# Kernel tuning notes

Measured on AMD Instinct MI355X. Metric: run time of the kernel, lower is better.

Reference implementation:

```python
import jax, jax.numpy as jnp
import numpy as np

B, C, N = 16, 256, 2048
CK = int(C * 0.25)  # key/query channels = 64
CV = C              # value_size = 1 -> value channels = C
BN_EPS = 1e-5


def setup_inputs() -> dict:
    key = jax.random.key(0)
    ks = jax.random.split(key, 7)
    sq = lambda fan_in: 1.0 / np.sqrt(fan_in)
    x = jax.random.normal(ks[0], (B, C, N), dtype=jnp.float32)
    # Conv1d(kernel_size=1, bias=False) weights stored as [out_ch, in_ch]
    Wq = jax.random.uniform(ks[1], (CK, C), jnp.float32, -sq(C), sq(C))
    Wk = jax.random.uniform(ks[2], (CK, C), jnp.float32, -sq(C), sq(C))
    Wv = jax.random.uniform(ks[3], (CV, C), jnp.float32, -sq(C), sq(C))
    Wl = jax.random.uniform(ks[4], (C, C), jnp.float32, -sq(C), sq(C))
    gamma = jnp.ones((C,), jnp.float32)
    beta = jnp.zeros((C,), jnp.float32)
    return {"x": x, "Wq": Wq, "Wk": Wk, "Wv": Wv, "Wl": Wl,
            "gamma": gamma, "beta": beta}


def reference(x, Wq, Wk, Wv, Wl, gamma, beta):
    # x: [B, C, N]
    q = jnp.einsum('oc,bcn->bno', Wq, x)   # [B, N, CK]  (q_conv then permute)
    k = jnp.einsum('oc,bcn->bon', Wk, x)   # [B, CK, N]
    v = jnp.einsum('oc,bcn->bno', Wv, x)   # [B, N, CV]  (v_conv then permute)

    w = jnp.einsum('bnk,bkm->bnm', q, k)   # [B, N, N] raw logits
    # NOTE: column-sum divisor uses RAW logits (RHS evaluated before reassignment
    # in the torch source), not the softmax output.
    col_sum = w.sum(axis=1, keepdims=True)                 # [B, 1, N]
    s = jax.nn.softmax(w, axis=-1) / (1e-9 + col_sum)      # [B, N, N]

    att = jnp.einsum('bnm,bmc->bcn', s, v)  # [B, C, N] (matmul + permute back)
    r = x - att                              # offset (residual of attention)

    # lbr: 1x1 conv -> BatchNorm1d (training-mode batch stats) -> ReLU
    h = jnp.einsum('oc,bcn->bon', Wl, r)     # [B, C, N]
    mean = h.mean(axis=(0, 2), keepdims=True)
    var = ((h - mean) ** 2).mean(axis=(0, 2), keepdims=True)  # biased, as BN
    hn = (h - mean) * jax.lax.rsqrt(var + BN_EPS)
    bn = hn * gamma[None, :, None] + beta[None, :, None]
    out = x + jax.nn.relu(bn)
    return out
```

## Files before the change

kernel.cpp:

```cpp
#include <hip/hip_runtime.h>

#define B_ 16
#define C_ 256
#define N_ 2048
#define CK_ 64

using f32x4  = __attribute__((ext_vector_type(4))) float;
using bf16x8 = __attribute__((ext_vector_type(8))) short;
using short4_t = __attribute__((ext_vector_type(4))) short;
using u32x2  = __attribute__((ext_vector_type(2))) unsigned;

static __device__ __forceinline__ float bf2f(short s){
  unsigned u = ((unsigned)(unsigned short)s) << 16;
  float f; __builtin_memcpy(&f, &u, 4); return f;
}
static __device__ __forceinline__ short f2bf(float f){
  unsigned u; __builtin_memcpy(&u, &f, 4);
  unsigned r = (u + 0x7fffu + ((u >> 16) & 1u)) >> 16;
  return (short)(unsigned short)r;
}

static __device__ __forceinline__ int vf_off(int cp, int ck){
  int q = cp >> 1; int ch = (((cp & 1) << 2) | ck) ^ (q & 7);
  return q*128 + ch*16;
}

__global__ void k_prep(const float* __restrict__ Wq, const float* __restrict__ Wk,
                       const float* __restrict__ Wv, const float* __restrict__ Wl,
                       short* __restrict__ Wb, short* __restrict__ Wlf,
                       const float* __restrict__ x, double* __restrict__ xsum){
  int bid = blockIdx.x;
  if(bid < 1024){
    int b = bid >> 6;
    int c = (bid & 63)*4 + (threadIdx.x>>6);
    int l = threadIdx.x & 63;
    const float* row = x + ((size_t)b*C_ + c)*N_;
    double s = 0.0;
    #pragma unroll
    for(int it = 0; it < 8; ++it){
      f32x4 v = *(const f32x4*)(row + it*256 + l*4);
      s += (double)v[0] + (double)v[1] + (double)v[2] + (double)v[3];
    }
    for(int off = 32; off; off >>= 1) s += __shfl_down(s, off);
    if(l == 0) xsum[b*C_ + c] = s;
  } else {
    int i = (bid - 1024)*256 + threadIdx.x;
    if(i < 384*C_){
      int o = i >> 8;
      float v;
      if(o < 64)       v = Wq[i];
      else if(o < 128) v = Wk[i - 64*C_];
      else             v = Wv[i - 128*C_];
      Wb[i] = f2bf(v);
    }
    if(i < C_*C_){
      int o = i >> 8, c = i & 255;
      int dest = (c>>5)*8192 + (o>>4)*512 + ((((c>>3)&3)*16) + (o&15))*8 + (c&7);
      Wlf[dest] = f2bf(Wl[i]);
    }
  }
}

__global__ void k_prep_g2(const double* __restrict__ xsum, const float* __restrict__ Wq,
                          const float* __restrict__ Wk, double* __restrict__ g){
  int b = blockIdx.x;
  __shared__ double xs[C_];
  __shared__ double t[CK_];
  int tid = threadIdx.x;
  xs[tid] = xsum[b*C_ + tid];
  __syncthreads();
  if(tid < CK_){
    double s = 0.0;
    const float* wr = Wq + (size_t)tid*C_;
    for(int c = 0; c < C_; ++c) s += (double)wr[c]*xs[c];
    t[tid] = s;
  }
  __syncthreads();
  double s = 0.0;
  for(int j = 0; j < CK_; ++j) s += (double)Wk[(size_t)j*C_ + tid]*t[j];
  g[b*C_ + tid] = s;
}

#define XROW 328
__global__ __launch_bounds__(256,2) void k_qkv(const float* __restrict__ x,
        const short* __restrict__ Wb, const double* __restrict__ gg,
        short* __restrict__ qbuf, short* __restrict__ kf, short* __restrict__ vf,
        short* __restrict__ xTb){
  int b = blockIdx.y; int n0 = blockIdx.x*64;
  int tid = threadIdx.x, w = tid>>6, l = tid&63, lo = l&15, g = l>>4;
  __shared__ __attribute__((aligned(16))) short xT[64*XROW];
  __shared__ double gs[C_];
  __shared__ double csum2[256][4];
  __shared__ float inv_lds[64];
  const float* xb = x + (size_t)b*C_*N_;
  gs[tid] = gg[b*C_ + tid];
  __syncthreads();
  int pp2 = tid >> 4, cg = tid & 15;
  double cs[4] = {0.0, 0.0, 0.0, 0.0};
  #pragma unroll
  for(int cc = 0; cc < 8; ++cc){
    int ci = cc*32 + 2*pp2;
    f32x4 x0 = *(const f32x4*)(xb + (size_t)ci*N_ + n0 + 4*cg);
    f32x4 x1 = *(const f32x4*)(xb + (size_t)(ci+1)*N_ + n0 + 4*cg);
    #pragma unroll
    for(int jq = 0; jq < 4; ++jq){
      cs[jq] += (double)x0[jq]*gs[ci] + (double)x1[jq]*gs[ci+1];
      unsigned pr = (unsigned)(unsigned short)f2bf(x0[jq])
                  | (((unsigned)(unsigned short)f2bf(x1[jq]))<<16);
      *(unsigned*)(&xT[(4*cg + jq)*XROW + cc*40 + 2*pp2]) = pr;
    }
  }
  csum2[tid][0] = cs[0]; csum2[tid][1] = cs[1];
  csum2[tid][2] = cs[2]; csum2[tid][3] = cs[3];
  __syncthreads();
  if(tid < 64){
    int cgq = tid >> 2, jq = tid & 3;
    double tot = 0.0;
    #pragma unroll
    for(int k = 0; k < 16; ++k) tot += csum2[k*16 + cgq][jq];
    inv_lds[tid] = (float)(1.0/(1e-9 + tot));
  }

  f32x4 acc[6][4];
  #pragma unroll
  for(int oi=0;oi<6;++oi) for(int nj=0;nj<4;++nj) acc[oi][nj]=(f32x4){0.f,0.f,0.f,0.f};
  int n2 = tid>>2, ii2 = tid&3;
  short* xtb = xTb + ((size_t)b*N_ + n0)*C_;
  #pragma unroll
  for(int cc = 0; cc < 8; ++cc){
    *(bf16x8*)(xtb + (size_t)n2*C_ + cc*32 + 8*ii2) =
        *(const bf16x8*)(&xT[n2*XROW + cc*40 + 8*ii2]);
    bf16x8 bfr[4];
    #pragma unroll
    for(int nj = 0; nj < 4; ++nj)
      bfr[nj] = *(const bf16x8*)(&xT[(nj*16 + lo)*XROW + cc*40 + 8*g]);
    #pragma unroll
    for(int oi = 0; oi < 6; ++oi){
      int o = w*96 + oi*16 + lo;
      bf16x8 af = *(const bf16x8*)(Wb + (size_t)o*C_ + cc*32 + 8*g);
      #pragma unroll
      for(int nj = 0; nj < 4; ++nj)
        acc[oi][nj] = __builtin_amdgcn_mfma_f32_16x16x32_bf16(af, bfr[nj], acc[oi][nj], 0,0,0);
    }
  }
  __syncthreads();

  short* qb  = qbuf + (size_t)b*N_*64;
  short* kfb = kf   + (size_t)b*N_*64;
  short* vfb = vf   + (size_t)b*C_*N_;
  #pragma unroll
  for(int oi = 0; oi < 6; ++oi){
    int obase = w*96 + oi*16;
    for(int nj = 0; nj < 4; ++nj){
      int n = n0 + nj*16 + lo;
      if(obase < 64){
        short4_t pk;
        #pragma unroll
        for(int r = 0; r < 4; ++r) pk[r] = f2bf(acc[oi][nj][r]);
        *(short4_t*)(qb + (size_t)n*64 + obase + 4*g) = pk;
      } else if(obase < 128){
        int C0 = obase - 64 + 4*g;
        int mt = (n0>>4) + nj;
        int h  = C0 >> 5;
        int lanep = ((C0>>3)&3)*16 + lo;
        short4_t pk;
        #pragma unroll
        for(int r = 0; r < 4; ++r) pk[r] = f2bf(acc[oi][nj][r]);
        *(short4_t*)(kfb + ((size_t)(mt*2 + h)*64 + lanep)*8 + (C0&4)) = pk;
      } else {
        float iv = inv_lds[nj*16 + lo];
        int ckk = (n>>3)&3, wi = n&7, mc = n>>5;
        #pragma unroll
        for(int r = 0; r < 4; ++r){
          int cp = obase - 128 + 4*g + r;
          vfb[(size_t)mc*8192 + (vf_off(cp, ckk)>>1) + wi] = f2bf(acc[oi][nj][r]*iv);
        }
      }
    }
  }
}
#undef XROW

__global__ __launch_bounds__(256,2) void k_attn(const short* __restrict__ qbuf,
        const short* __restrict__ kf, const short* __restrict__ vf,
        short* __restrict__ att){
  int d = blockIdx.x;
  int xcd = d & 7, j = d >> 3;
  int b = xcd*2 + (j >> 5);
  int n0 = (j & 31)*64;
  int tid = threadIdx.x;
  int w = tid>>6, l = tid&63, lo = l&15, g = l>>4;

  __shared__ short vlds[2][16384];
  __shared__ short plds[4096];
  __shared__ float rs_lds[64];

  const short* qb  = qbuf + (size_t)b*N_*64;
  const short* kfb = kf   + (size_t)b*N_*64;
  const short* vfb = vf   + (size_t)b*C_*N_;

  bf16x8 qa0, qa1;
  {
    const short* qrow = qb + (size_t)(n0 + w*16 + lo)*64;
    qa0 = *(const bf16x8*)(qrow + 8*g);
    qa1 = *(const bf16x8*)(qrow + 32 + 8*g);
  }
  int paoff[4][2], bvoff[4][2], pw[4];
  #pragma unroll
  for(int rt = 0; rt < 4; ++rt)
    #pragma unroll
    for(int mh = 0; mh < 2; ++mh)
      paoff[rt][mh] = (rt*16 + lo)*128 + (((mh*4 + g) ^ (lo&7))*16);
  #pragma unroll
  for(int jj = 0; jj < 4; ++jj)
    #pragma unroll
    for(int mh = 0; mh < 2; ++mh)
      bvoff[jj][mh] = mh*16384 + vf_off(w*64 + jj*16 + lo, g);
  #pragma unroll
  for(int tt = 0; tt < 4; ++tt)
    pw[tt] = (w*16 + lo)*128 + (((tt*2 + (g>>1)) ^ (lo&7))*16) + (g&1)*8;

  const short* kl   = kfb + l*8;
  const short* vsrc = vfb + w*2048 + l*8;

  f32x4 oacc[4][4];
  #pragma unroll
  for(int rt=0;rt<4;++rt) for(int jj=0;jj<4;++jj) oacc[rt][jj]=(f32x4){0.f,0.f,0.f,0.f};
  float srow = 0.f;

  bf16x8 kA0,kA1,kA2,kA3,kA4,kA5,kA6,kA7;
  bf16x8 kB0,kB1,kB2,kB3,kB4,kB5,kB6,kB7;

#define LOADK(S, MC) { const short* kp = kl + (size_t)((MC)&31)*4096; \
    k##S##0 = *(const bf16x8*)(kp);        k##S##1 = *(const bf16x8*)(kp + 512); \
    k##S##2 = *(const bf16x8*)(kp + 1024); k##S##3 = *(const bf16x8*)(kp + 1536); \
    k##S##4 = *(const bf16x8*)(kp + 2048); k##S##5 = *(const bf16x8*)(kp + 2560); \
    k##S##6 = *(const bf16x8*)(kp + 3072); k##S##7 = *(const bf16x8*)(kp + 3584); }
#define GLLDS(SRC, DST) __builtin_amdgcn_global_load_lds( \
    (const __attribute__((address_space(1))) void*)(SRC), \
    (__attribute__((address_space(3))) void*)(DST), 16, 0, 0)
#define VDMA(MC, NB) { const short* vs = vsrc + (size_t)(2*(MC))*8192; \
    char* dst = (char*)&vlds[NB][0] + w*4096; \
    GLLDS(vs,        dst);        GLLDS(vs +  512, dst + 1024); \
    GLLDS(vs + 1024, dst + 2048); GLLDS(vs + 1536, dst + 3072); \
    GLLDS(vs + 8192,  dst + 16384); GLLDS(vs + 8704,  dst + 17408); \
    GLLDS(vs + 9216,  dst + 18432); GLLDS(vs + 9728,  dst + 19456); }
#define QKT(S, TT, KE, KO) { \
    f32x4 a = (f32x4){0.f,0.f,0.f,0.f}; \
    a = __builtin_amdgcn_mfma_f32_16x16x32_bf16(k##S##KE, qa0, a, 0,0,0); \
    a = __builtin_amdgcn_mfma_f32_16x16x32_bf16(k##S##KO, qa1, a, 0,0,0); \
    float e[4]; \
    _Pragma("unroll") \
    for(int r = 0; r < 4; ++r) e[r] = __builtin_exp2f(fmaf(a[r], 1.44269504f, -17.3123405f)); \
    srow += e[0]+e[1]+e[2]+e[3]; \
    unsigned p0, p1; \
    asm("v_cvt_pk_bf16_f32 %0, %1, %2" : "=v"(p0) : "v"(e[0]), "v"(e[1])); \
    asm("v_cvt_pk_bf16_f32 %0, %1, %2" : "=v"(p1) : "v"(e[2]), "v"(e[3])); \
    { u32x2 pv = {p0, p1}; *(u32x2*)((char*)&plds[0] + pw[TT]) = pv; } }

  LOADK(A, 0);
  LOADK(B, 1);
  VDMA(0, 0);

#define BODY(BUF, S, MC) { \
    VDMA(((MC)+1)&31, (BUF)^1); \
    QKT(S, 0, 0, 1); QKT(S, 1, 2, 3); QKT(S, 2, 4, 5); QKT(S, 3, 6, 7); \
    LOADK(S, (MC)+2); \
    __builtin_amdgcn_sched_barrier(0); \
    asm volatile("s_waitcnt vmcnt(16) lgkmcnt(0)" ::: "memory"); \
    __builtin_amdgcn_s_barrier(); \
    __builtin_amdgcn_sched_barrier(0); \
    __builtin_amdgcn_s_setprio(1); \
    _Pragma("unroll") \
    for(int mh = 0; mh < 2; ++mh){ \
      bf16x8 pa[4], bv[4]; \
      _Pragma("unroll") \
      for(int rt = 0; rt < 4; ++rt) pa[rt] = *(const bf16x8*)((char*)&plds[0] + paoff[rt][mh]); \
      _Pragma("unroll") \
      for(int jj = 0; jj < 4; ++jj) bv[jj] = *(const bf16x8*)((char*)&vlds[BUF][0] + bvoff[jj][mh]); \
      _Pragma("unroll") \
      for(int rt = 0; rt < 4; ++rt) \
        _Pragma("unroll") \
        for(int jj = 0; jj < 4; ++jj) \
          oacc[rt][jj] = __builtin_amdgcn_mfma_f32_16x16x32_bf16(pa[rt], bv[jj], oacc[rt][jj], 0,0,0); \
    } \
    __builtin_amdgcn_s_setprio(0); \
    __builtin_amdgcn_sched_barrier(0); \
    asm volatile("s_waitcnt lgkmcnt(0)" ::: "memory"); \
    __builtin_amdgcn_s_barrier(); \
    __builtin_amdgcn_sched_barrier(0); }

  #pragma unroll 1
  for(int it = 0; it < 16; ++it){
    BODY(0, A, 2*it);
    BODY(1, B, 2*it + 1);
  }
#undef BODY
#undef QKT
#undef VDMA
#undef GLLDS
#undef LOADK

  float S = srow;
  S += __shfl_xor(S, 16);
  S += __shfl_xor(S, 32);
  if(l < 16) rs_lds[w*16 + l] = 1.f/(S + 1e-30f);
  __syncthreads();
  float rinvs[4][4];
  #pragma unroll
  for(int rt = 0; rt < 4; ++rt)
    #pragma unroll
    for(int r = 0; r < 4; ++r) rinvs[rt][r] = rs_lds[rt*16 + 4*g + r];

  short* attb = att + (size_t)b*N_*C_;
  #pragma unroll
  for(int rt = 0; rt < 4; ++rt)
    #pragma unroll
    for(int jj = 0; jj < 4; ++jj)
      #pragma unroll
      for(int r = 0; r < 4; ++r){
        int n = n0 + rt*16 + 4*g + r;
        int c = w*64 + jj*16 + lo;
        attb[(size_t)n*C_ + c] = f2bf(oacc[rt][jj][r]*rinvs[rt][r]);
      }
}

__global__ __launch_bounds__(256,2) void k_hgemm(const short* __restrict__ xTb,
        const short* __restrict__ att, const short* __restrict__ Wlf,
        short* __restrict__ hT, float* __restrict__ part){
  int b = blockIdx.y; int n0 = blockIdx.x*64;
  int bid = b*32 + blockIdx.x;
  int tid = threadIdx.x, w = tid>>6, l = tid&63, lo = l&15, g = l>>4;
  __shared__ __attribute__((aligned(16))) short rT[64*C_];
  const short* xtb = xTb + ((size_t)b*N_ + n0)*C_;
  const short* atb = att + ((size_t)b*N_ + n0)*C_;
  int half = l >> 5, ch = l & 31;
  #pragma unroll
  for(int k = 0; k < 8; ++k){
    int n = k*8 + w*2 + half;
    size_t off = (size_t)n*C_ + ch*8;
    bf16x8 xv = *(const bf16x8*)(xtb + off);
    bf16x8 av = *(const bf16x8*)(atb + off);
    bf16x8 rv;
    #pragma unroll
    for(int jq = 0; jq < 8; ++jq) rv[jq] = f2bf(bf2f(xv[jq]) - bf2f(av[jq]));
    *(bf16x8*)(&rT[n*C_ + ((ch ^ (n&7))*8)]) = rv;
  }
  __syncthreads();

  f32x4 acc[4][4];
  #pragma unroll
  for(int ot=0;ot<4;++ot) for(int nj=0;nj<4;++nj) acc[ot][nj]=(f32x4){0.f,0.f,0.f,0.f};
  #pragma unroll
  for(int cb = 0; cb < 8; ++cb){
    bf16x8 bfr[4];
    #pragma unroll
    for(int nj = 0; nj < 4; ++nj)
      bfr[nj] = *(const bf16x8*)(&rT[(nj*16 + lo)*C_ + (((cb*4 + g) ^ (lo&7))*8)]);
    #pragma unroll
    for(int ot = 0; ot < 4; ++ot){
      bf16x8 af = *(const bf16x8*)(Wlf + ((size_t)(cb*16 + w*4 + ot))*512 + l*8);
      #pragma unroll
      for(int nj = 0; nj < 4; ++nj)
        acc[ot][nj] = __builtin_amdgcn_mfma_f32_16x16x32_bf16(af, bfr[nj], acc[ot][nj], 0,0,0);
    }
  }
  float* pr_ = part + (size_t)bid*512;
  #pragma unroll
  for(int ot = 0; ot < 4; ++ot){
    float s4[4] = {0,0,0,0}, q4[4] = {0,0,0,0};
    for(int nj = 0; nj < 4; ++nj)
      #pragma unroll
      for(int r = 0; r < 4; ++r){ float v = acc[ot][nj][r]; s4[r] += v; q4[r] += v*v; }
    #pragma unroll
    for(int r = 0; r < 4; ++r){
      float ss = s4[r], qq = q4[r];
      for(int msk = 1; msk < 16; msk <<= 1){ ss += __shfl_xor(ss, msk); qq += __shfl_xor(qq, msk); }
      if(lo == 0){
        int o = w*64 + ot*16 + 4*g + r;
        pr_[o] = ss;
        pr_[256 + o] = qq;
      }
    }
  }
  __syncthreads();
  #pragma unroll
  for(int ot = 0; ot < 4; ++ot)
    #pragma unroll
    for(int nj = 0; nj < 4; ++nj)
      #pragma unroll
      for(int r = 0; r < 4; ++r){
        int o = w*64 + ot*16 + 4*g + r;
        int n = nj*16 + lo;
        rT[o*64 + (n ^ (((o>>2)&3)*16))] = f2bf(acc[ot][nj][r]);
      }
  __syncthreads();
  short* hTb = hT + (size_t)b*C_*N_ + n0;
  {
    int ro = tid >> 3, li = tid & 7;
    #pragma unroll
    for(int pss = 0; pss < 8; ++pss){
      int o = pss*32 + ro;
      bf16x8 v = *(const bf16x8*)(&rT[o*64 + ((li*8) ^ (((o>>2)&3)*16))]);
      *(bf16x8*)(hTb + (size_t)o*N_ + li*8) = v;
    }
  }
}

__global__ void k_bnred(const float* __restrict__ part, float* __restrict__ part2){
  int j = blockIdx.x;
  int t = threadIdx.x;
  float s0 = 0.f, s1 = 0.f;
  #pragma unroll
  for(int r = 0; r < 8; ++r){
    const float* pr_ = part + (size_t)(j*8 + r)*512;
    s0 += pr_[t];
    s1 += pr_[t + 256];
  }
  part2[(size_t)j*512 + t] = s0;
  part2[(size_t)j*512 + t + 256] = s1;
}

__global__ void k_bnfin(const float* __restrict__ part2,
                        const float* __restrict__ gamma, const float* __restrict__ beta,
                        float* __restrict__ bnsc, float* __restrict__ bnsh){
  __shared__ float ls[4][512];
  int t = threadIdx.x; int o = t & 255, seg = t >> 8;
  float s = 0.f, q = 0.f;
  for(int r = seg*16; r < seg*16 + 16; ++r){
    s += part2[(size_t)r*512 + o];
    q += part2[(size_t)r*512 + 256 + o];
  }
  ls[seg][o] = s; ls[seg][256 + o] = q;
  __syncthreads();
  if(t < 256){
    float S = ls[0][t] + ls[1][t] + ls[2][t] + ls[3][t];
    float Q = ls[0][256+t] + ls[1][256+t] + ls[2][256+t] + ls[3][256+t];
    float cnt = (float)(B_*N_);
    float mean = S/cnt;
    float var  = Q/cnt - mean*mean;
    float is   = rsqrtf(var + 1e-5f);
    float sc   = gamma[t]*is;
    bnsc[t] = sc;
    bnsh[t] = beta[t] - mean*sc;
  }
}

__global__ void k_final(const float* __restrict__ x, const short* __restrict__ hT,
                        const float* __restrict__ bnsc, const float* __restrict__ bnsh,
                        float* __restrict__ out){
  int row = blockIdx.x;
  int c = row & 255;
  float sc = bnsc[c], sh = bnsh[c];
  const short* hr = hT + (size_t)row*N_;
  const float* xr = x + (size_t)row*N_;
  float* orow = out + (size_t)row*N_;
  int t = threadIdx.x;
  bf16x8 hv = *(const bf16x8*)(hr + t*8);
  f32x4 x0 = *(const f32x4*)(xr + t*8);
  f32x4 x1 = *(const f32x4*)(xr + t*8 + 4);
  f32x4 o0, o1;
  #pragma unroll
  for(int jq = 0; jq < 4; ++jq){
    o0[jq] = x0[jq] + fmaxf(fmaf(bf2f(hv[jq]), sc, sh), 0.f);
    o1[jq] = x1[jq] + fmaxf(fmaf(bf2f(hv[jq+4]), sc, sh), 0.f);
  }
  *(f32x4*)(orow + t*8) = o0;
  *(f32x4*)(orow + t*8 + 4) = o1;
}

extern "C" void kernel_launch(void* const* d_in, const int* in_sizes, int n_in,
                              void* d_out, int out_size, void* d_ws, size_t ws_size,
                              hipStream_t stream){
  const float* x     = (const float*)d_in[0];
  const float* Wq    = (const float*)d_in[1];
  const float* Wk    = (const float*)d_in[2];
  const float* Wv    = (const float*)d_in[3];
  const float* Wl    = (const float*)d_in[4];
  const float* gamma = (const float*)d_in[5];
  const float* beta  = (const float*)d_in[6];
  float* out = (float*)d_out;

  char* p = (char*)d_ws;
  double* g    = (double*)p; p += (size_t)B_*C_*8;
  double* xsum = (double*)p; p += (size_t)B_*C_*8;
  short* Wb   = (short*)p;  p += (size_t)384*C_*2;
  short* Wlf  = (short*)p;  p += (size_t)C_*C_*2;
  short* qbuf = (short*)p;  p += (size_t)B_*N_*64*2;
  short* kf   = (short*)p;  p += (size_t)B_*N_*64*2;
  short* vf   = (short*)p;  p += (size_t)B_*C_*N_*2;
  short* xTb  = (short*)p;  p += (size_t)B_*N_*C_*2;
  short* att  = (short*)p;  p += (size_t)B_*N_*C_*2;
  float* part = (float*)p;  p += (size_t)512*512*4;
  float* part2= (float*)p;  p += (size_t)64*512*4;
  float* bnsc = (float*)p;  p += C_*4;
  float* bnsh = (float*)p;  p += C_*4;
  short* hT = vf;

  k_prep   <<<1408, 256, 0, stream>>>(Wq, Wk, Wv, Wl, Wb, Wlf, x, xsum);
  k_prep_g2<<<B_, 256, 0, stream>>>(xsum, Wq, Wk, g);
  k_qkv    <<<dim3(N_/64, B_), 256, 0, stream>>>(x, Wb, g, qbuf, kf, vf, xTb);
  k_attn   <<<512, 256, 0, stream>>>(qbuf, kf, vf, att);
  k_hgemm  <<<dim3(N_/64, B_), 256, 0, stream>>>(xTb, att, Wlf, hT, part);
  k_bnred  <<<64, 256, 0, stream>>>(part, part2);
  k_bnfin  <<<1, 1024, 0, stream>>>(part2, gamma, beta, bnsc, bnsh);
  k_final  <<<4096, 256, 0, stream>>>(x, hT, bnsc, bnsh, out);
}
```

Baseline: 130.7 us.

## Fuse residual and Wl GEMM epilogue into attention kernel

The attention kernel now keeps its normalized output tile in LDS, subtracts it from the transposed x, runs the Wl projection with MFMA, writes BN partial sums and stores the h tile directly. This removes the separate k_hgemm launch and the global write and read of the attention buffer. hT gets its own workspace buffer because vf is still being read by other attention blocks. It adds register pressure and a longer epilogue to an already heavy kernel, which may hurt occupancy or scheduling.

```diff
diff --git a/kernel.cpp b/kernel.cpp
--- a/kernel.cpp
+++ b/kernel.cpp
@@ -183,7 +183,8 @@
 
 __global__ __launch_bounds__(256,2) void k_attn(const short* __restrict__ qbuf,
         const short* __restrict__ kf, const short* __restrict__ vf,
-        short* __restrict__ att){
+        const short* __restrict__ xTb, const short* __restrict__ Wlf,
+        short* __restrict__ hT, float* __restrict__ part){
   int d = blockIdx.x;
   int xcd = d & 7, j = d >> 3;
   int b = xcd*2 + (j >> 5);
@@ -305,6 +306,7 @@
   S += __shfl_xor(S, 16);
   S += __shfl_xor(S, 32);
   if(l < 16) rs_lds[w*16 + l] = 1.f/(S + 1e-30f);
+  asm volatile("s_waitcnt vmcnt(0)" ::: "memory");
   __syncthreads();
   float rinvs[4][4];
   #pragma unroll
@@ -312,45 +314,36 @@
     #pragma unroll
     for(int r = 0; r < 4; ++r) rinvs[rt][r] = rs_lds[rt*16 + 4*g + r];
 
-  short* attb = att + (size_t)b*N_*C_;
+  short* rT = (short*)&vlds[0][0];
   #pragma unroll
   for(int rt = 0; rt < 4; ++rt)
     #pragma unroll
     for(int jj = 0; jj < 4; ++jj)
       #pragma unroll
       for(int r = 0; r < 4; ++r){
-        int n = n0 + rt*16 + 4*g + r;
+        int nloc = rt*16 + 4*g + r;
         int c = w*64 + jj*16 + lo;
-        attb[(size_t)n*C_ + c] = f2bf(oacc[rt][jj][r]*rinvs[rt][r]);
+        rT[nloc*C_ + (((c>>3) ^ (nloc&7))*8 + (c&7))] = f2bf(oacc[rt][jj][r]*rinvs[rt][r]);
       }
-}
-
-__global__ __launch_bounds__(256,2) void k_hgemm(const short* __restrict__ xTb,
-        const short* __restrict__ att, const short* __restrict__ Wlf,
-        short* __restrict__ hT, float* __restrict__ part){
-  int b = blockIdx.y; int n0 = blockIdx.x*64;
-  int bid = b*32 + blockIdx.x;
-  int tid = threadIdx.x, w = tid>>6, l = tid&63, lo = l&15, g = l>>4;
-  __shared__ __attribute__((aligned(16))) short rT[64*C_];
-  const short* xtb = xTb + ((size_t)b*N_ + n0)*C_;
-  const short* atb = att + ((size_t)b*N_ + n0)*C_;
-  int half = l >> 5, ch = l & 31;
-  #pragma unroll
-  for(int k = 0; k < 8; ++k){
-    int n = k*8 + w*2 + half;
-    size_t off = (size_t)n*C_ + ch*8;
-    bf16x8 xv = *(const bf16x8*)(xtb + off);
-    bf16x8 av = *(const bf16x8*)(atb + off);
-    bf16x8 rv;
-    #pragma unroll
-    for(int jq = 0; jq < 8; ++jq) rv[jq] = f2bf(bf2f(xv[jq]) - bf2f(av[jq]));
-    *(bf16x8*)(&rT[n*C_ + ((ch ^ (n&7))*8)]) = rv;
-  }
-  __syncthreads();
-
-  f32x4 acc[4][4];
-  #pragma unroll
-  for(int ot=0;ot<4;++ot) for(int nj=0;nj<4;++nj) acc[ot][nj]=(f32x4){0.f,0.f,0.f,0.f};
+  __syncthreads();
+  {
+    const short* xtb = xTb + ((size_t)b*N_ + n0)*C_;
+    int half = l >> 5, ch = l & 31;
+    #pragma unroll
+    for(int k = 0; k < 8; ++k){
+      int n = k*8 + w*2 + half;
+      bf16x8 xv = *(const bf16x8*)(xtb + (size_t)n*C_ + ch*8);
+      bf16x8* pr = (bf16x8*)(&rT[n*C_ + ((ch ^ (n&7))*8)]);
+      bf16x8 av = *pr, rv;
+      #pragma unroll
+      for(int jq = 0; jq < 8; ++jq) rv[jq] = f2bf(bf2f(xv[jq]) - bf2f(av[jq]));
+      *pr = rv;
+    }
+  }
+  __syncthreads();
+  f32x4 acc2[4][4];
+  #pragma unroll
+  for(int ot=0;ot<4;++ot) for(int nj=0;nj<4;++nj) acc2[ot][nj]=(f32x4){0.f,0.f,0.f,0.f};
   #pragma unroll
   for(int cb = 0; cb < 8; ++cb){
     bf16x8 bfr[4];
@@ -362,16 +355,17 @@
       bf16x8 af = *(const bf16x8*)(Wlf + ((size_t)(cb*16 + w*4 + ot))*512 + l*8);
       #pragma unroll
       for(int nj = 0; nj < 4; ++nj)
-        acc[ot][nj] = __builtin_amdgcn_mfma_f32_16x16x32_bf16(af, bfr[nj], acc[ot][nj], 0,0,0);
-    }
-  }
+        acc2[ot][nj] = __builtin_amdgcn_mfma_f32_16x16x32_bf16(af, bfr[nj], acc2[ot][nj], 0,0,0);
+    }
+  }
+  int bid = b*32 + (n0 >> 6);
   float* pr_ = part + (size_t)bid*512;
   #pragma unroll
   for(int ot = 0; ot < 4; ++ot){
     float s4[4] = {0,0,0,0}, q4[4] = {0,0,0,0};
     for(int nj = 0; nj < 4; ++nj)
       #pragma unroll
-      for(int r = 0; r < 4; ++r){ float v = acc[ot][nj][r]; s4[r] += v; q4[r] += v*v; }
+      for(int r = 0; r < 4; ++r){ float v = acc2[ot][nj][r]; s4[r] += v; q4[r] += v*v; }
     #pragma unroll
     for(int r = 0; r < 4; ++r){
       float ss = s4[r], qq = q4[r];
@@ -383,7 +377,7 @@
       }
     }
   }
-  __syncthreads();
+  short* tT = (short*)&vlds[1][0];
   #pragma unroll
   for(int ot = 0; ot < 4; ++ot)
     #pragma unroll
@@ -392,7 +386,7 @@
       for(int r = 0; r < 4; ++r){
         int o = w*64 + ot*16 + 4*g + r;
         int n = nj*16 + lo;
-        rT[o*64 + (n ^ (((o>>2)&3)*16))] = f2bf(acc[ot][nj][r]);
+        tT[o*64 + (n ^ (((o>>2)&3)*16))] = f2bf(acc2[ot][nj][r]);
       }
   __syncthreads();
   short* hTb = hT + (size_t)b*C_*N_ + n0;
@@ -401,7 +395,7 @@
     #pragma unroll
     for(int pss = 0; pss < 8; ++pss){
       int o = pss*32 + ro;
-      bf16x8 v = *(const bf16x8*)(&rT[o*64 + ((li*8) ^ (((o>>2)&3)*16))]);
+      bf16x8 v = *(const bf16x8*)(&tT[o*64 + ((li*8) ^ (((o>>2)&3)*16))]);
       *(bf16x8*)(hTb + (size_t)o*N_ + li*8) = v;
     }
   }
@@ -490,18 +484,16 @@
   short* kf   = (short*)p;  p += (size_t)B_*N_*64*2;
   short* vf   = (short*)p;  p += (size_t)B_*C_*N_*2;
   short* xTb  = (short*)p;  p += (size_t)B_*N_*C_*2;
-  short* att  = (short*)p;  p += (size_t)B_*N_*C_*2;
+  short* hT   = (short*)p;  p += (size_t)B_*N_*C_*2;
   float* part = (float*)p;  p += (size_t)512*512*4;
   float* part2= (float*)p;  p += (size_t)64*512*4;
   float* bnsc = (float*)p;  p += C_*4;
   float* bnsh = (float*)p;  p += C_*4;
-  short* hT = vf;
 
   k_prep   <<<1408, 256, 0, stream>>>(Wq, Wk, Wv, Wl, Wb, Wlf, x, xsum);
   k_prep_g2<<<B_, 256, 0, stream>>>(xsum, Wq, Wk, g);
   k_qkv    <<<dim3(N_/64, B_), 256, 0, stream>>>(x, Wb, g, qbuf, kf, vf, xTb);
-  k_attn   <<<512, 256, 0, stream>>>(qbuf, kf, vf, att);
-  k_hgemm  <<<dim3(N_/64, B_), 256, 0, stream>>>(xTb, att, Wlf, hT, part);
+  k_attn   <<<512, 256, 0, stream>>>(qbuf, kf, vf, xTb, Wlf, hT, part);
   k_bnred  <<<64, 256, 0, stream>>>(part, part2);
   k_bnfin  <<<1, 1024, 0, stream>>>(part2, gamma, beta, bnsc, bnsh);
   k_final  <<<4096, 256, 0, stream>>>(x, hT, bnsc, bnsh, out);
```

Result: faster. 123.3 us (-5.6%).
